# Kernel tuning notes

Measured on AMD Instinct MI355X. Metric: run time of the kernel, lower is better.

The kernel has to match this reference:

```python
import jax, jax.numpy as jnp
import numpy as np
import math

B, S, D, H, DFF, NB = 16, 512, 512, 8, 2048, 2
DK = D // H
L = 3 * NB  # NB blocks_1 layers + 2*NB blocks_2 layers
NEG = -1e32
LN_EPS = 1e-5


def _layernorm(x, g, b):
    mu = jnp.mean(x, -1, keepdims=True)
    var = jnp.mean((x - mu) ** 2, -1, keepdims=True)
    return (x - mu) * jax.lax.rsqrt(var + LN_EPS) * g + b


def _attention(q, k, v, mask, gamma, zero_pad):
    # q,k,v: [B,H,S,DK]; mask: [S,S] bool; gamma: [H]
    scores = jnp.einsum('bhid,bhjd->bhij', q, k) / math.sqrt(DK)
    maskf = mask.astype(scores.dtype)
    # no-grad distance-decay block (torch.no_grad + .detach())
    p = jax.nn.softmax(jnp.where(mask, scores, NEG), axis=-1) * maskf
    distcum = jnp.cumsum(p, axis=-1)
    disttot = jnp.sum(p, axis=-1, keepdims=True)
    idx = jnp.arange(S, dtype=scores.dtype)
    pos = jnp.abs(idx[None, :] - idx[:, None])  # |i-j|, [S,S]
    dist = jnp.sqrt(jnp.clip((disttot - distcum) * pos, 0.0, None))
    dist = jax.lax.stop_gradient(dist)
    g = -jax.nn.softplus(gamma)[None, :, None, None]  # [1,H,1,1]
    total_effect = jnp.clip(jnp.exp(dist * g), 1e-5, 1e5)
    scores = jnp.where(mask, scores * total_effect, NEG)
    attn = jax.nn.softmax(scores, axis=-1)
    if zero_pad:
        attn = attn.at[:, :, 0, :].set(0.0)
    return jnp.einsum('bhij,bhjd->bhid', attn, v)


def _mha(q, k, v, mask, zero_pad, Wk, bk, Wv, bv, Wo, bo, gam):
    # kq_same=True: queries also use the k projection
    def proj(x, W, b):
        return (x @ W + b).reshape(B, S, H, DK).transpose(0, 2, 1, 3)
    qh = proj(q, Wk, bk)
    kh = proj(k, Wk, bk)
    vh = proj(v, Wv, bv)
    out = _attention(qh, kh, vh, mask, gam, zero_pad)
    out = out.transpose(0, 2, 1, 3).reshape(B, S, D)
    return out @ Wo + bo


def _layer(mask_flag, query, key_, values, apply_pos, p):
    (Wk, bk, Wv, bv, Wo, bo, gam, g1, bn1, W1, bf1, W2, bf2, g2, bn2) = p
    idx = jnp.arange(S)
    if mask_flag == 1:
        mask = idx[None, :] <= idx[:, None]  # peek current + past
    else:
        mask = idx[None, :] < idx[:, None]   # strictly past
    zero_pad = (mask_flag == 0)
    q2 = _mha(query, key_, values, mask, zero_pad, Wk, bk, Wv, bv, Wo, bo, gam)
    query = _layernorm(query + q2, g1, bn1)
    if apply_pos:
        q2 = jax.nn.relu(query @ W1 + bf1) @ W2 + bf2
        query = _layernorm(query + q2, g2, bn2)
    return query


def _forward(q_embed_data, qa_embed_data, pid_embed_data, params):
    # emb_type='qid' (no 'pdiff') -> pid_embed_data unused inside attention
    def pslice(l):
        return tuple(a[l] for a in params)
    y = qa_embed_data
    x = q_embed_data
    for l in range(NB):  # blocks_1: self-attn on y, mask=1
        y = _layer(1, y, y, y, True, pslice(l))
    for i in range(NB):  # blocks_2: alternating (mask=1, no FFN) / (mask=0, values=y)
        x = _layer(1, x, x, x, False, pslice(NB + 2 * i))
        x = _layer(0, x, x, y, True, pslice(NB + 2 * i + 1))
    return x, y


def setup_inputs() -> dict:
    key = jax.random.key(0)
    ks = jax.random.split(key, 10)
    sD = 1.0 / math.sqrt(D)
    sF = 1.0 / math.sqrt(DFF)
    f32 = jnp.float32
    return {
        'q_embed_data': jax.random.normal(ks[0], (B, S, D), f32),
        'qa_embed_data': jax.random.normal(ks[1], (B, S, D), f32),
        'pid_embed_data': jax.random.normal(ks[2], (B, S, D), f32),
        'Wk': jax.random.normal(ks[3], (L, D, D), f32) * sD,
        'bk': jnp.zeros((L, D), f32),
        'Wv': jax.random.normal(ks[4], (L, D, D), f32) * sD,
        'bv': jnp.zeros((L, D), f32),
        'Wo': jax.random.normal(ks[5], (L, D, D), f32) * sD,
        'bo': jnp.zeros((L, D), f32),
        'gammas': jax.random.normal(ks[6], (L, H), f32) * 0.5,
        'ln1_g': jnp.ones((L, D), f32),
        'ln1_b': jnp.zeros((L, D), f32),
        'W1': jax.random.normal(ks[7], (L, D, DFF), f32) * sD,
        'b1': jnp.zeros((L, DFF), f32),
        'W2': jax.random.normal(ks[8], (L, DFF, D), f32) * sF,
        'b2': jnp.zeros((L, D), f32),
        'ln2_g': jnp.ones((L, D), f32),
        'ln2_b': jnp.zeros((L, D), f32),
    }


def reference(q_embed_data, qa_embed_data, pid_embed_data, Wk, bk, Wv, bv, Wo, bo,
              gammas, ln1_g, ln1_b, W1, b1, W2, b2, ln2_g, ln2_b):
    params = (Wk, bk, Wv, bv, Wo, bo, gammas, ln1_g, ln1_b, W1, b1, W2, b2, ln2_g, ln2_b)
    x, y = _forward(q_embed_data, qa_embed_data, pid_embed_data, params)
    return (x, y)
```

## Files before the change

kernel.cpp:

```cpp
#include <hip/hip_runtime.h>
#include <hip/hip_bf16.h>

#define Bsz  16
#define Sl   512
#define Dm   512
#define Hn   8
#define DKh  64
#define DFFn 2048
#define MROWS (Bsz * Sl)
#define NEGV (-1e32f)

typedef _Float16 f16;
typedef f16 f16x8 __attribute__((ext_vector_type(8)));
typedef f16 f16x4 __attribute__((ext_vector_type(4)));
typedef float f32x4 __attribute__((ext_vector_type(4)));

#define GLDS16(g, l) __builtin_amdgcn_global_load_lds( \
    (const __attribute__((address_space(1))) void*)(g), \
    (__attribute__((address_space(3))) void*)(l), 16, 0, 0)

struct PrepArgs {
    const float *Wk, *Wv, *Wo, *W1, *W2, *bk, *bv, *q_emb, *qa_emb;
    f16 *wkvh, *woh, *w1h, *w2h;
    float *bkv, *xbuf, *ybuf;
    f16 *xh, *yh;
};

__device__ __forceinline__ void wconv_body(const float* src, f16* dst,
        int K, int N, int lmap, size_t zstride, int z, int nx, int ny,
        int t, float (*T)[36])
{
    int ls = lmap ? (z < 2 ? z : 2 * z - 1) : z;
    const float* S = src + (size_t)ls * K * N;
    f16* Dt = dst + (size_t)z * zstride;
    int n0 = nx * 32, k0 = ny * 32;
    int r = t >> 3, c = (t & 7) * 4;
    float4 v = *(const float4*)(S + (size_t)(k0 + r) * N + n0 + c);
    T[r][c] = v.x; T[r][c + 1] = v.y; T[r][c + 2] = v.z; T[r][c + 3] = v.w;
    __syncthreads();
    int n = t >> 3, kq = (t & 7) * 4;
    f16x4 o = { (f16)T[kq][n], (f16)T[kq + 1][n], (f16)T[kq + 2][n], (f16)T[kq + 3][n] };
    *(f16x4*)(Dt + (size_t)(n0 + n) * K + k0 + kq) = o;
}

__global__ __launch_bounds__(256) void k_prep(PrepArgs a)
{
    __shared__ float T[32][36];
    int id = blockIdx.x;
    int t = threadIdx.x;
    const size_t WDD = (size_t)Dm * Dm;
    const size_t WDF = (size_t)Dm * DFFn;
    const size_t WKV = 2 * WDD;

    if (id < 4608) {
        int which = id / 1536, rest = id % 1536;
        int z = rest >> 8, r2 = rest & 255;
        int nx = r2 & 15, ny = r2 >> 4;
        if (which == 0)      wconv_body(a.Wk, a.wkvh,       Dm, Dm, 0, WKV, z, nx, ny, t, T);
        else if (which == 1) wconv_body(a.Wv, a.wkvh + WDD, Dm, Dm, 0, WKV, z, nx, ny, t, T);
        else                 wconv_body(a.Wo, a.woh,        Dm, Dm, 0, WDD, z, nx, ny, t, T);
    } else if (id < 8704) {
        int id2 = id - 4608;
        int z = id2 >> 10, r2 = id2 & 1023;
        int nx = r2 & 63, ny = r2 >> 6;
        wconv_body(a.W1, a.w1h, Dm, DFFn, 1, WDF, z, nx, ny, t, T);
    } else if (id < 12800) {
        int id3 = id - 8704;
        int z = id3 >> 10, r2 = id3 & 1023;
        int nx = r2 & 15, ny = r2 >> 4;
        wconv_body(a.W2, a.w2h, DFFn, Dm, 1, WDF, z, nx, ny, t, T);
    } else if (id < 12824) {
        int i = (id - 12800) * 256 + t;
        int z = i >> 10, c = i & 1023;
        a.bkv[i] = (c < 512) ? a.bk[z * 512 + c] : a.bv[z * 512 + c - 512];
    } else if (id < 29208) {
        int i = (id - 12824) * 256 + t;
        float v = a.q_emb[i];
        a.xbuf[i] = v; a.xh[i] = (f16)v;
    } else {
        int i = (id - 29208) * 256 + t;
        float v = a.qa_emb[i];
        a.ybuf[i] = v; a.yh[i] = (f16)v;
    }
}

template <int RELU, int OUT16, int VTOUT, int BK64>
__global__ __launch_bounds__(256) void k_gemm(
    const f16* __restrict__ A, const f16* __restrict__ Bt,
    const float* __restrict__ bias, float* __restrict__ C, f16* __restrict__ Ch,
    int M, int N, int K,
    const f16* __restrict__ A2, f16* __restrict__ Ch2)
{
    constexpr int HL = BK64 ? 2 : 1;
    constexpr int BUF = HL * 4096;
    __shared__ f16 As[2 * BUF];
    __shared__ f16 Bs[2 * BUF];
    int tid = threadIdx.x;
    int w = tid >> 6, lane = tid & 63;
    int ln = lane & 15, rg = lane >> 4;
    int wr = w >> 1, wc = w & 1;
    int m0 = blockIdx.y * 128;
    int half = (VTOUT == 3) ? (blockIdx.x >> 2) : 0;
    int n0 = (VTOUT == 3) ? (blockIdx.x & 3) * 128 : blockIdx.x * 128;

    const f16* Ause = (VTOUT == 3 && half) ? A2 : A;
    const f16* Btuse = (VTOUT == 3) ? Bt + (size_t)half * 512 * 512 : Bt;
    const float* biasuse = (VTOUT == 3) ? bias + half * 512 : bias;

    int s0 = tid, s1 = 256 + tid;
    int r0s = s0 >> 2, c0s = ((s0 & 3) ^ ((s0 >> 3) & 3));
    int r1s = s1 >> 2, c1s = ((s1 & 3) ^ ((s1 >> 3) & 3));

    const f16* a0 = Ause + (size_t)(m0 + r0s) * K + c0s * 8;
    const f16* a1 = Ause + (size_t)(m0 + r1s) * K + c1s * 8;
    const f16* b0 = Btuse + (size_t)(n0 + r0s) * K + c0s * 8;
    const f16* b1 = Btuse + (size_t)(n0 + r1s) * K + c1s * 8;

    int cc8 = (rg ^ ((ln >> 1) & 3)) * 8;

    f32x4 acc[4][4] = {};

    int nk = K >> (BK64 ? 6 : 5);

    auto STAGE = [&](int nb, int kt) {
        f16* lA = As + nb * BUF + w * 512;
        f16* lB = Bs + nb * BUF + w * 512;
        GLDS16(a0 + kt, lA);
        GLDS16(a1 + kt, lA + 2048);
        GLDS16(b0 + kt, lB);
        GLDS16(b1 + kt, lB + 2048);
        if (BK64) {
            GLDS16(a0 + kt + 32, lA + 4096);
            GLDS16(a1 + kt + 32, lA + 4096 + 2048);
            GLDS16(b0 + kt + 32, lB + 4096);
            GLDS16(b1 + kt + 32, lB + 4096 + 2048);
        }
    };

    STAGE(0, 0);
    __syncthreads();

    int cur = 0;
    for (int t = 0; t < nk; ++t) {
        if (t + 1 < nk) STAGE(cur ^ 1, (t + 1) << (BK64 ? 6 : 5));

#pragma unroll
        for (int hh = 0; hh < HL; ++hh) {
            const f16* Ab = As + cur * BUF + hh * 4096;
            const f16* Bb = Bs + cur * BUF + hh * 4096;
            f16x8 af[4], bf[4];
#pragma unroll
            for (int i = 0; i < 4; ++i) {
                int m = wr * 64 + i * 16 + ln;
                af[i] = *(const f16x8*)(Ab + m * 32 + cc8);
                int nn = wc * 64 + i * 16 + ln;
                bf[i] = *(const f16x8*)(Bb + nn * 32 + cc8);
            }
#pragma unroll
            for (int i = 0; i < 4; ++i)
#pragma unroll
                for (int j = 0; j < 4; ++j)
                    acc[i][j] = __builtin_amdgcn_mfma_f32_16x16x32_f16(af[i], bf[j], acc[i][j], 0, 0, 0);
        }

        __syncthreads();
        cur ^= 1;
    }

#pragma unroll
    for (int j = 0; j < 4; ++j) {
        int col = n0 + wc * 64 + j * 16 + ln;
        float bj = biasuse[col];
#pragma unroll
        for (int i = 0; i < 4; ++i) {
            int rb = m0 + wr * 64 + i * 16 + rg * 4;
            if (VTOUT == 1) {
                int bq = rb >> 9, s = rb & 511;
                int hh = col >> 6, dk = col & 63;
                f16x4 o;
#pragma unroll
                for (int r = 0; r < 4; ++r) o[r] = (f16)(acc[i][j][r] + bj);
                *(f16x4*)(Ch + (((size_t)(bq * 8 + hh) * 64 + dk) << 9) + s) = o;
            } else if (VTOUT == 2) {
                if (n0 < 512) {
#pragma unroll
                    for (int r = 0; r < 4; ++r)
                        Ch[(size_t)(rb + r) * 512 + col] = (f16)(acc[i][j][r] + bj);
                } else {
                    f16* Cv = (f16*)C;
                    int colv = col - 512;
                    int bq = rb >> 9, s = rb & 511;
                    int hh = colv >> 6, dk = colv & 63;
                    f16x4 o;
#pragma unroll
                    for (int r = 0; r < 4; ++r) o[r] = (f16)(acc[i][j][r] + bj);
                    *(f16x4*)(Cv + (((size_t)(bq * 8 + hh) * 64 + dk) << 9) + s) = o;
                }
            } else if (VTOUT == 3) {
                if (half == 0) {
#pragma unroll
                    for (int r = 0; r < 4; ++r)
                        Ch[(size_t)(rb + r) * 512 + col] = (f16)(acc[i][j][r] + bj);
                } else {
                    int bq = rb >> 9, s = rb & 511;
                    int hh = col >> 6, dk = col & 63;
                    f16x4 o;
#pragma unroll
                    for (int r = 0; r < 4; ++r) o[r] = (f16)(acc[i][j][r] + bj);
                    *(f16x4*)(Ch2 + (((size_t)(bq * 8 + hh) * 64 + dk) << 9) + s) = o;
                }
            } else {
#pragma unroll
                for (int r = 0; r < 4; ++r) {
                    float v = acc[i][j][r] + bj;
                    if (RELU) v = fmaxf(v, 0.f);
                    if (OUT16) Ch[(size_t)(rb + r) * N + col] = (f16)v;
                    else       C [(size_t)(rb + r) * N + col] = v;
                }
            }
        }
    }
}

template <int JTC>
__device__ __forceinline__ void attn_body(
    float (*Sc)[516], f16* Ph, const f16* Qbase, const f16* vbase, f16* ob,
    f16x8 aq0, f16x8 aq1, float g,
    int w, int lane, int ln, int rg, int i0, int maskflag)
{
#pragma unroll
    for (int ui = 0; ui < JTC; ++ui) {
        int u = w + ui * 4;
        const f16* kb = Qbase + (size_t)(u * 16 + ln) * Dm + rg * 8;
        f16x8 b0 = *(const f16x8*)(kb);
        f16x8 b1 = *(const f16x8*)(kb + 32);
        f32x4 c = {};
        c = __builtin_amdgcn_mfma_f32_16x16x32_f16(aq0, b0, c, 0, 0, 0);
        c = __builtin_amdgcn_mfma_f32_16x16x32_f16(aq1, b1, c, 0, 0, 0);
#pragma unroll
        for (int r = 0; r < 4; ++r)
            Sc[rg * 4 + r][u * 16 + ln] = c[r];
    }
    __syncthreads();

    int jbase = lane * JTC;
    int im = i0 + w * 4;

    float ss[4][JTC];
    float run[4];
#pragma unroll
    for (int q = 0; q < 4; ++q) {
        const float* Srow = &Sc[w * 4 + q][0];
        if constexpr (JTC == 8) {
            float4 t0 = *(const float4*)(Srow + jbase);
            float4 t1 = *(const float4*)(Srow + jbase + 4);
            ss[q][0] = t0.x; ss[q][1] = t0.y; ss[q][2] = t0.z; ss[q][3] = t0.w;
            ss[q][4] = t1.x; ss[q][5] = t1.y; ss[q][6] = t1.z; ss[q][7] = t1.w;
        } else if constexpr (JTC == 4) {
            float4 t0 = *(const float4*)(Srow + jbase);
            ss[q][0] = t0.x; ss[q][1] = t0.y; ss[q][2] = t0.z; ss[q][3] = t0.w;
        } else {
#pragma unroll
            for (int k = 0; k < JTC; ++k) ss[q][k] = Srow[jbase + k];
        }
        int jmax = maskflag ? (im + q) : (im + q - 1);
        float acc = 0.f;
#pragma unroll
        for (int k = 0; k < JTC; ++k) {
            int j = jbase + k;
            float s = (j <= jmax) ? ss[q][k] * 0.125f : NEGV;
            ss[q][k] = s;
            acc += __expf(s);
        }
        run[q] = acc;
    }
    float sl[4] = { run[0], run[1], run[2], run[3] };
#pragma unroll
    for (int off = 1; off < 64; off <<= 1) {
        float n0 = __shfl_up(sl[0], off);
        float n1 = __shfl_up(sl[1], off);
        float n2 = __shfl_up(sl[2], off);
        float n3 = __shfl_up(sl[3], off);
        if (lane >= off) { sl[0] += n0; sl[1] += n1; sl[2] += n2; sl[3] += n3; }
    }

    float Z2[4];
#pragma unroll
    for (int q = 0; q < 4; ++q) {
        float excl = sl[q] - run[q];
        float Z = __shfl(sl[q], 63);
        float inv = 1.f / Z;
        int i = im + q;
        float csum = 0.f, z2 = 0.f;
#pragma unroll
        for (int k = 0; k < JTC; ++k) {
            int j = jbase + k;
            float s = ss[q][k];
            csum += __expf(s);
            float rem = (Z - excl - csum) * inv;
            float pos = fabsf((float)(i - j));
            float dd = fmaxf(rem * pos, 0.f);
            float te = __expf(sqrtf(dd) * g);
            te = fminf(fmaxf(te, 1e-5f), 1e5f);
            float pe2 = __expf(s * te);
            ss[q][k] = pe2;
            z2 += pe2;
        }
        Z2[q] = z2;
    }
#pragma unroll
    for (int off = 32; off >= 1; off >>= 1) {
        Z2[0] += __shfl_xor(Z2[0], off);
        Z2[1] += __shfl_xor(Z2[1], off);
        Z2[2] += __shfl_xor(Z2[2], off);
        Z2[3] += __shfl_xor(Z2[3], off);
    }
    __syncthreads();

#pragma unroll
    for (int q = 0; q < 4; ++q) {
        int r = w * 4 + q;
        float inv2 = 1.f / Z2[q];
        int zp = (maskflag == 0) && (im + q == 0);
        if constexpr (JTC == 8) {
            int slot = (lane & ~7) | ((lane & 7) ^ (r & 7));
            f16x8 o8;
#pragma unroll
            for (int k = 0; k < 8; ++k)
                o8[k] = (f16)(zp ? 0.f : ss[q][k] * inv2);
            *(f16x8*)(Ph + r * 512 + slot * 8) = o8;
        } else if constexpr (JTC == 4) {
            int cj = lane >> 1;
            int slot = (cj & ~7) | ((cj & 7) ^ (r & 7));
            f16x4 o4;
#pragma unroll
            for (int k = 0; k < 4; ++k)
                o4[k] = (f16)(zp ? 0.f : ss[q][k] * inv2);
            *(f16x4*)(Ph + r * 512 + slot * 8 + (lane & 1) * 4) = o4;
        } else {
#pragma unroll
            for (int k = 0; k < JTC; ++k) {
                int j = jbase + k;
                int cj = j >> 3;
                int slot = (cj & ~7) | ((cj & 7) ^ (r & 7));
                Ph[r * 512 + slot * 8 + (j & 7)] =
                    (f16)(zp ? 0.f : ss[q][k] * inv2);
            }
        }
    }
    __syncthreads();

    f32x4 oa0 = {}, oa1 = {};
#pragma unroll
    for (int f = 0; f < 2 * JTC; ++f) {
        f16x8 bv = *(const f16x8*)(vbase + (f >> 1) * 64 + (f & 1) * 32);
        int c = (f >> 1) * 8 + (f & 1) * 4 + rg;
        int slot = (c & ~7) | ((c & 7) ^ (ln & 7));
        f16x8 ap = *(const f16x8*)(Ph + ln * 512 + slot * 8);
        if (f & 1) oa1 = __builtin_amdgcn_mfma_f32_16x16x32_f16(ap, bv, oa1, 0, 0, 0);
        else       oa0 = __builtin_amdgcn_mfma_f32_16x16x32_f16(ap, bv, oa0, 0, 0, 0);
    }
    f32x4 oa = oa0 + oa1;
#pragma unroll
    for (int r = 0; r < 4; ++r)
        ob[(size_t)r * Dm] = (f16)oa[r];
}

__global__ __launch_bounds__(256, 4) void k_attn(
    const f16* __restrict__ Qh, const f16* __restrict__ VT,
    f16* __restrict__ O, const float* __restrict__ gam, int maskflag)
{
    __shared__ float Sc[16][516];
    f16* Ph = (f16*)Sc;

    int tid = threadIdx.x;
    int w = tid >> 6, lane = tid & 63;
    int ln = lane & 15, rg = lane >> 4;

    int bid = blockIdx.x;
    int lbid = (bid & 7) * 512 + (bid >> 3);
    int tile = 31 - (lbid & 31);
    int bh = lbid >> 5;
    int b = bh >> 3, h = bh & 7;
    int i0 = tile * 16;
    int jtc = (tile >> 2) + 1;

    const f16* Qbase = Qh + ((size_t)b * Sl) * Dm + h * DKh;
    const f16* vbase = VT + ((size_t)bh * 64 + w * 16 + ln) * 512 + rg * 8;
    f16* ob = O + ((size_t)b * Sl + i0 + rg * 4) * Dm + h * DKh + w * 16 + ln;

    float gm = gam[h];
    float g = -((gm > 20.f) ? gm : log1pf(__expf(gm)));

    f16x8 aq0 = *(const f16x8*)(Qbase + (size_t)(i0 + ln) * Dm + rg * 8);
    f16x8 aq1 = *(const f16x8*)(Qbase + (size_t)(i0 + ln) * Dm + 32 + rg * 8);

    switch (jtc) {
    case 1: attn_body<1>(Sc, Ph, Qbase, vbase, ob, aq0, aq1, g, w, lane, ln, rg, i0, maskflag); break;
    case 2: attn_body<2>(Sc, Ph, Qbase, vbase, ob, aq0, aq1, g, w, lane, ln, rg, i0, maskflag); break;
    case 3: attn_body<3>(Sc, Ph, Qbase, vbase, ob, aq0, aq1, g, w, lane, ln, rg, i0, maskflag); break;
    case 4: attn_body<4>(Sc, Ph, Qbase, vbase, ob, aq0, aq1, g, w, lane, ln, rg, i0, maskflag); break;
    case 5: attn_body<5>(Sc, Ph, Qbase, vbase, ob, aq0, aq1, g, w, lane, ln, rg, i0, maskflag); break;
    case 6: attn_body<6>(Sc, Ph, Qbase, vbase, ob, aq0, aq1, g, w, lane, ln, rg, i0, maskflag); break;
    case 7: attn_body<7>(Sc, Ph, Qbase, vbase, ob, aq0, aq1, g, w, lane, ln, rg, i0, maskflag); break;
    default: attn_body<8>(Sc, Ph, Qbase, vbase, ob, aq0, aq1, g, w, lane, ln, rg, i0, maskflag); break;
    }
}

__global__ __launch_bounds__(256) void k_ln(
    const float* __restrict__ Xn, const float* __restrict__ Rr,
    const float* __restrict__ gw, const float* __restrict__ bw,
    float* __restrict__ Out, f16* __restrict__ Outh)
{
    int tid = threadIdx.x;
    int w = tid >> 6, lane = tid & 63;
    int row = blockIdx.x * 4 + w;
    const float* xr = Xn + (size_t)row * Dm;
    const float* rr = Rr + (size_t)row * Dm;
    int c0 = lane * 4, c1 = 256 + lane * 4;
    float4 va = *(const float4*)(xr + c0);
    float4 vb = *(const float4*)(xr + c1);
    float4 ra = *(const float4*)(rr + c0);
    float4 rb = *(const float4*)(rr + c1);
    va.x += ra.x; va.y += ra.y; va.z += ra.z; va.w += ra.w;
    vb.x += rb.x; vb.y += rb.y; vb.z += rb.z; vb.w += rb.w;
    float sum = va.x + va.y + va.z + va.w + vb.x + vb.y + vb.z + vb.w;
#pragma unroll
    for (int off = 32; off >= 1; off >>= 1) sum += __shfl_xor(sum, off);
    float mu = sum * (1.f / 512.f);
    float var = 0.f;
    {
        float d;
        d = va.x - mu; var += d * d;  d = va.y - mu; var += d * d;
        d = va.z - mu; var += d * d;  d = va.w - mu; var += d * d;
        d = vb.x - mu; var += d * d;  d = vb.y - mu; var += d * d;
        d = vb.z - mu; var += d * d;  d = vb.w - mu; var += d * d;
    }
#pragma unroll
    for (int off = 32; off >= 1; off >>= 1) var += __shfl_xor(var, off);
    float rs = rsqrtf(var * (1.f / 512.f) + 1e-5f);
    float4 ga = *(const float4*)(gw + c0);
    float4 gb = *(const float4*)(gw + c1);
    float4 ba = *(const float4*)(bw + c0);
    float4 bb = *(const float4*)(bw + c1);
    float4 oa, ob;
    oa.x = (va.x - mu) * rs * ga.x + ba.x;  oa.y = (va.y - mu) * rs * ga.y + ba.y;
    oa.z = (va.z - mu) * rs * ga.z + ba.z;  oa.w = (va.w - mu) * rs * ga.w + ba.w;
    ob.x = (vb.x - mu) * rs * gb.x + bb.x;  ob.y = (vb.y - mu) * rs * gb.y + bb.y;
    ob.z = (vb.z - mu) * rs * gb.z + bb.z;  ob.w = (vb.w - mu) * rs * gb.w + bb.w;
    float* orow = Out + (size_t)row * Dm;
    f16* ohrow = Outh + (size_t)row * Dm;
    *(float4*)(orow + c0) = oa;
    *(float4*)(orow + c1) = ob;
    f16x4 ha = { (f16)oa.x, (f16)oa.y, (f16)oa.z, (f16)oa.w };
    f16x4 hb = { (f16)ob.x, (f16)ob.y, (f16)ob.z, (f16)ob.w };
    *(f16x4*)(ohrow + c0) = ha;
    *(f16x4*)(ohrow + c1) = hb;
}

extern "C" void kernel_launch(void* const* d_in, const int* in_sizes, int n_in,
                              void* d_out, int out_size, void* d_ws, size_t ws_size,
                              hipStream_t stream)
{
    const float* q_emb  = (const float*)d_in[0];
    const float* qa_emb = (const float*)d_in[1];
    const float* Wk  = (const float*)d_in[3];
    const float* bk  = (const float*)d_in[4];
    const float* Wv  = (const float*)d_in[5];
    const float* bv  = (const float*)d_in[6];
    const float* Wo  = (const float*)d_in[7];
    const float* bo  = (const float*)d_in[8];
    const float* gam = (const float*)d_in[9];
    const float* l1g = (const float*)d_in[10];
    const float* l1b = (const float*)d_in[11];
    const float* W1  = (const float*)d_in[12];
    const float* b1  = (const float*)d_in[13];
    const float* W2  = (const float*)d_in[14];
    const float* b2  = (const float*)d_in[15];
    const float* l2g = (const float*)d_in[16];
    const float* l2b = (const float*)d_in[17];
    float* outp = (float*)d_out;

    const size_t NE  = (size_t)MROWS * Dm;
    const size_t WDD = (size_t)Dm * Dm;
    const size_t WDF = (size_t)Dm * DFFn;
    const size_t WKV = 2 * WDD;

    float* xbuf = (float*)d_ws;
    float* ybuf = xbuf + NE;
    float* t2   = ybuf + NE;
    f16* xh  = (f16*)(t2 + NE);
    f16* yh  = xh + NE;
    f16* R   = yh + NE;
    f16* qh  = R;
    f16* vt  = R + 2 * NE;
    f16* t1h = R + 3 * NE;
    f16* fbh = R;
    f16* wkvh = R + 4 * NE;
    f16* woh = wkvh + 6 * WKV;
    f16* w1h = woh + 6 * WDD;
    f16* w2h = w1h + 4 * WDF;
    float* bkv = (float*)(w2h + 4 * WDF);

    PrepArgs pa;
    pa.Wk = Wk; pa.Wv = Wv; pa.Wo = Wo; pa.W1 = W1; pa.W2 = W2;
    pa.bk = bk; pa.bv = bv; pa.q_emb = q_emb; pa.qa_emb = qa_emb;
    pa.wkvh = wkvh; pa.woh = woh; pa.w1h = w1h; pa.w2h = w2h;
    pa.bkv = bkv; pa.xbuf = xbuf; pa.ybuf = ybuf; pa.xh = xh; pa.yh = yh;
    k_prep<<<45592, 256, 0, stream>>>(pa);

    auto layer = [&](int l, int maskflag, float* Xq, f16* Xqh, f16* Xvh,
                     bool apply_pos, float* finalOut) {
        if (Xqh == Xvh) {
            k_gemm<0, 1, 2, 1><<<dim3(1024 / 128, MROWS / 128), 256, 0, stream>>>(
                Xqh, wkvh + (size_t)l * WKV, bkv + l * 1024, (float*)vt, qh,
                MROWS, 1024, Dm, nullptr, nullptr);
        } else {
            k_gemm<0, 1, 3, 1><<<dim3(8, MROWS / 128), 256, 0, stream>>>(
                Xqh, wkvh + (size_t)l * WKV, bkv + l * 1024, nullptr, qh,
                MROWS, 512, Dm, Xvh, vt);
        }
        k_attn<<<Bsz * Hn * 32, 256, 0, stream>>>(qh, vt, t1h, gam + l * Hn, maskflag);
        k_gemm<0, 0, 0, 1><<<dim3(Dm / 128, MROWS / 128), 256, 0, stream>>>(
            t1h, woh + (size_t)l * WDD, bo + l * Dm, t2, nullptr,
            MROWS, Dm, Dm, nullptr, nullptr);
        if (apply_pos) {
            k_ln<<<MROWS / 4, 256, 0, stream>>>(t2, Xq, l1g + l * Dm, l1b + l * Dm, Xq, Xqh);
            int sl = (l < 2) ? l : ((l + 1) >> 1);
            k_gemm<1, 1, 0, 0><<<dim3(DFFn / 128, MROWS / 128), 256, 0, stream>>>(
                Xqh, w1h + (size_t)sl * WDF, b1 + l * DFFn, nullptr, fbh,
                MROWS, DFFn, Dm, nullptr, nullptr);
            k_gemm<0, 0, 0, 1><<<dim3(Dm / 128, MROWS / 128), 256, 0, stream>>>(
                fbh, w2h + (size_t)sl * WDF, b2 + l * Dm, t2, nullptr,
                MROWS, Dm, DFFn, nullptr, nullptr);
            k_ln<<<MROWS / 4, 256, 0, stream>>>(t2, Xq, l2g + l * Dm, l2b + l * Dm,
                                                finalOut ? finalOut : Xq, Xqh);
        } else {
            k_ln<<<MROWS / 4, 256, 0, stream>>>(t2, Xq, l1g + l * Dm, l1b + l * Dm,
                                                finalOut ? finalOut : Xq, Xqh);
        }
    };

    const size_t NEo = NE;
    layer(0, 1, ybuf, yh, yh, true, nullptr);
    layer(1, 1, ybuf, yh, yh, true, outp + NEo);
    layer(2, 1, xbuf, xh, xh, false, nullptr);
    layer(3, 0, xbuf, xh, yh, true, nullptr);
    layer(4, 1, xbuf, xh, xh, false, nullptr);
    layer(5, 0, xbuf, xh, yh, true, outp);
}
```

Baseline: 1.106 ms.

## Triple-buffer BK64 GEMM LDS pipeline with partial vmcnt waits

```diff
diff --git a/kernel.cpp b/kernel.cpp
--- a/kernel.cpp
+++ b/kernel.cpp
@@ -93,8 +93,9 @@
 {
     constexpr int HL = BK64 ? 2 : 1;
     constexpr int BUF = HL * 4096;
-    __shared__ f16 As[2 * BUF];
-    __shared__ f16 Bs[2 * BUF];
+    constexpr int NBUF = BK64 ? 3 : 2;
+    __shared__ f16 As[NBUF * BUF];
+    __shared__ f16 Bs[NBUF * BUF];
     int tid = threadIdx.x;
     int w = tid >> 6, lane = tid & 63;
     int ln = lane & 15, rg = lane >> 4;
@@ -106,6 +107,12 @@
     const f16* Ause = (VTOUT == 3 && half) ? A2 : A;
     const f16* Btuse = (VTOUT == 3) ? Bt + (size_t)half * 512 * 512 : Bt;
     const float* biasuse = (VTOUT == 3) ? bias + half * 512 : bias;
+
+    float bj4[4];
+#pragma unroll
+    for (int j = 0; j < 4; ++j)
+        bj4[j] = biasuse[n0 + wc * 64 + j * 16 + ln];
+    if (BK64) asm volatile("s_waitcnt vmcnt(0)" ::: "memory");
 
     int s0 = tid, s1 = 256 + tid;
     int r0s = s0 >> 2, c0s = ((s0 & 3) ^ ((s0 >> 3) & 3));
@@ -137,17 +144,11 @@
         }
     };
 
-    STAGE(0, 0);
-    __syncthreads();
-
-    int cur = 0;
-    for (int t = 0; t < nk; ++t) {
-        if (t + 1 < nk) STAGE(cur ^ 1, (t + 1) << (BK64 ? 6 : 5));
-
+    auto COMPUTE = [&](int nb) {
 #pragma unroll
         for (int hh = 0; hh < HL; ++hh) {
-            const f16* Ab = As + cur * BUF + hh * 4096;
-            const f16* Bb = Bs + cur * BUF + hh * 4096;
+            const f16* Ab = As + nb * BUF + hh * 4096;
+            const f16* Bb = Bs + nb * BUF + hh * 4096;
             f16x8 af[4], bf[4];
 #pragma unroll
             for (int i = 0; i < 4; ++i) {
@@ -162,15 +163,41 @@
                 for (int j = 0; j < 4; ++j)
                     acc[i][j] = __builtin_amdgcn_mfma_f32_16x16x32_f16(af[i], bf[j], acc[i][j], 0, 0, 0);
         }
-
+    };
+
+    if (BK64) {
+        STAGE(0, 0);
+        STAGE(1, 64);
+        asm volatile("s_waitcnt vmcnt(8)" ::: "memory");
+        __builtin_amdgcn_s_barrier();
+        int cur = 0;
+        for (int t = 0; t < nk; ++t) {
+            int nx = t + 2;
+            if (nx < nk) STAGE(cur == 0 ? 2 : cur - 1, nx << 6);
+            COMPUTE(cur);
+            if (t + 1 < nk) {
+                if (nx < nk) asm volatile("s_waitcnt vmcnt(8)" ::: "memory");
+                else         asm volatile("s_waitcnt vmcnt(0)" ::: "memory");
+                __builtin_amdgcn_s_barrier();
+            }
+            cur = (cur == 2) ? 0 : cur + 1;
+        }
+    } else {
+        STAGE(0, 0);
         __syncthreads();
-        cur ^= 1;
+        int cur = 0;
+        for (int t = 0; t < nk; ++t) {
+            if (t + 1 < nk) STAGE(cur ^ 1, (t + 1) << 5);
+            COMPUTE(cur);
+            __syncthreads();
+            cur ^= 1;
+        }
     }
 
 #pragma unroll
     for (int j = 0; j < 4; ++j) {
         int col = n0 + wc * 64 + j * 16 + ln;
-        float bj = biasuse[col];
+        float bj = bj4[j];
 #pragma unroll
         for (int i = 0; i < 4; ++i) {
             int rb = m0 + wr * 64 + i * 16 + rg * 4;
```

Result: slower. 1.237 ms (+11.8%).
